# Optimization experiments

Measured on AMD Instinct MI355X. Metric: run time of the kernel, lower is better.

Reference implementation:

```python
import jax, jax.numpy as jnp
import numpy as np

B, D = 4096, 256          # event batch, message dim
N_NODES = 100000
N_COMM = 2000             # community_max_num
M = 128                   # max_member_num
N_ACTIVE = 1500           # currently active communities (community_index)


def setup_inputs() -> dict:
    key = jax.random.key(0)
    ks = jax.random.split(key, 8)
    return {
        "unique_message": jax.random.normal(ks[0], (B, D), jnp.float32),
        "member_score": jax.random.uniform(ks[1], (N_COMM, M), jnp.float32),
        "timestamps": jax.random.uniform(ks[2], (B,), jnp.float32) * 1e4,
        "nodes": jax.random.randint(ks[3], (B,), 0, N_NODES),
        "node2community": jax.random.randint(ks[4], (N_NODES,), 0, N_COMM),
        "community2node": jax.random.randint(ks[5], (N_COMM, M), 0, N_NODES),
        "member_num": jax.random.randint(ks[6], (N_COMM,), 1, M + 1),
        "community_index": jax.random.randint(ks[7], (N_ACTIVE,), 0, N_COMM),
    }


def reference(unique_message, member_score, timestamps, nodes,
              node2community, community2node, member_num, community_index):
    # community of each event node: [B]
    cids = node2community[nodes]
    # use_index: event's community is among active communities (== .any in torch code)
    use = (cids[None, :] == community_index[:, None]).any(axis=0)  # [B]

    # Ragged per-community gather, expressed as padded+masked dense ops.
    ms = member_score[cids]          # [B, M] scores of the event's community members
    mnum = member_num[cids]          # [B]   valid member count per event
    pos = jnp.arange(M)
    valid = (pos[None, :] < mnum[:, None]) & use[:, None]  # [B, M] mask = ragged prefix

    # outer product member_score[:mnum] x message  (torch.mm(score.view(-1,1), msg.view(1,-1)))
    messages = jnp.where(valid[:, :, None],
                         ms[:, :, None] * unique_message[:, None, :],
                         0.0)                                # [B, M, D]
    upd_nodes = jnp.where(valid, community2node[cids], -1)   # [B, M] (-1 = pad)
    upd_ts = jnp.where(valid, timestamps[:, None], 0.0)      # [B, M]
    return messages, upd_nodes, upd_ts
```

## Files before the change

### kernel.cpp

```cpp
#include <hip/hip_runtime.h>
#include <hip/hip_bf16.h>


__global__ void scatter_mask_kernel(const int* __restrict__ cidx,
                                    int* __restrict__ mask, int n) {
    int i = blockIdx.x * blockDim.x + threadIdx.x;
    if (i < n) mask[cidx[i]] = 1;
}

__global__ __launch_bounds__(256) void topk_comm_main_kernel(
    const float* __restrict__ unique_message,
    const float* __restrict__ member_score,
    const float* __restrict__ timestamps,
    const int*   __restrict__ nodes,
    const int*   __restrict__ node2community,
    const int*   __restrict__ community2node,
    const int*   __restrict__ member_num,
    const int*   __restrict__ mask,
    float* __restrict__ out_msgs,
    float* __restrict__ out_nodes,
    float* __restrict__ out_ts,
    int M)
{
    const int b   = blockIdx.x;
    const int tid = threadIdx.x;

    const int  cid  = node2community[nodes[b]];
    const bool use  = (mask[cid] != 0);
    const int  mnum = member_num[cid];
    const float tsb = timestamps[b];

    const int c = tid & 63;
    const int r = tid >> 6;

    const float4 m4 =
        reinterpret_cast<const float4*>(unique_message + (size_t)b * 256)[c];

    float4* __restrict__ outm =
        reinterpret_cast<float4*>(out_msgs + (size_t)b * M * 256);
    const float* __restrict__ ms_row = member_score + (size_t)cid * M;

    for (int m = r; m < M; m += 4) {
        const bool valid = use && (m < mnum);
        const float s = valid ? ms_row[m] : 0.0f;
        float4 o;
        o.x = s * m4.x; o.y = s * m4.y; o.z = s * m4.z; o.w = s * m4.w;
        outm[(size_t)m * 64 + c] = o;
    }

    const int* __restrict__ c2n_row = community2node + (size_t)cid * M;
    for (int m = tid; m < M; m += 256) {
        const bool valid = use && (m < mnum);
        out_nodes[(size_t)b * M + m] = valid ? (float)c2n_row[m] : -1.0f;
        out_ts[(size_t)b * M + m]    = valid ? tsb : 0.0f;
    }
}

extern "C" void kernel_launch(void* const* d_in, const int* in_sizes, int n_in,
                              void* d_out, int out_size, void* d_ws, size_t ws_size,
                              hipStream_t stream) {
    const float* unique_message = (const float*)d_in[0];
    const float* member_score   = (const float*)d_in[1];
    const float* timestamps     = (const float*)d_in[2];
    const int*   nodes          = (const int*)d_in[3];
    const int*   node2community = (const int*)d_in[4];
    const int*   community2node = (const int*)d_in[5];
    const int*   member_num     = (const int*)d_in[6];
    const int*   community_index= (const int*)d_in[7];

    const int B        = in_sizes[2];
    const int N_COMM   = in_sizes[6];
    const int M        = in_sizes[1] / N_COMM;
    const int N_ACTIVE = in_sizes[7];

    int* mask = (int*)d_ws;
    hipMemsetAsync(mask, 0, (size_t)N_COMM * sizeof(int), stream);
    scatter_mask_kernel<<<(N_ACTIVE + 255) / 256, 256, 0, stream>>>(
        community_index, mask, N_ACTIVE);

    float* out_msgs  = (float*)d_out;
    float* out_nodes = out_msgs + (size_t)B * M * 256;
    float* out_ts    = out_nodes + (size_t)B * M;

    topk_comm_main_kernel<<<B, 256, 0, stream>>>(
        unique_message, member_score, timestamps, nodes,
        node2community, community2node, member_num, mask,
        out_msgs, out_nodes, out_ts, M);
}
```

Before: 116.7 us.

## Fuse active-community check into main kernel and use nontemporal stores

Removes the memset and scatter-mask launches; each block scans community_index itself with a wave vote to decide membership. Member scores are staged in shared memory, M and D are fixed at compile time, the member loop is fully unrolled with contiguous per-wave row ranges, and all outputs use nontemporal stores. This cuts launch overhead and keeps streaming writes out of cache, but every block now rereads the active list, and the hardcoded dimensions only suit this shape.

```diff
diff --git a/kernel.cpp b/kernel.cpp
--- a/kernel.cpp
+++ b/kernel.cpp
@@ -2,13 +2,12 @@
 #include <hip/hip_bf16.h>
 
 
-__global__ void scatter_mask_kernel(const int* __restrict__ cidx,
-                                    int* __restrict__ mask, int n) {
-    int i = blockIdx.x * blockDim.x + threadIdx.x;
-    if (i < n) mask[cidx[i]] = 1;
-}
+typedef float f32x4 __attribute__((ext_vector_type(4)));
 
-__global__ __launch_bounds__(256) void topk_comm_main_kernel(
+constexpr int Dc = 256;
+constexpr int Mc = 128;
+
+__global__ __launch_bounds__(256) void topk_main_spec(
     const float* __restrict__ unique_message,
     const float* __restrict__ member_score,
     const float* __restrict__ timestamps,
@@ -16,74 +15,90 @@
     const int*   __restrict__ node2community,
     const int*   __restrict__ community2node,
     const int*   __restrict__ member_num,
-    const int*   __restrict__ mask,
+    const int*   __restrict__ community_index,
+    int n_active,
     float* __restrict__ out_msgs,
     float* __restrict__ out_nodes,
-    float* __restrict__ out_ts,
-    int M)
+    float* __restrict__ out_ts)
 {
     const int b   = blockIdx.x;
     const int tid = threadIdx.x;
 
-    const int  cid  = node2community[nodes[b]];
-    const bool use  = (mask[cid] != 0);
-    const int  mnum = member_num[cid];
-    const float tsb = timestamps[b];
+    __shared__ float s_score[Mc];
+    __shared__ int   s_use;
+
+    const int   cid  = node2community[nodes[b]];
+    const int   mnum = member_num[cid];
+    const float tsb  = timestamps[b];
+
+    if (tid == 0) s_use = 0;
+    __syncthreads();
+
+    bool found = false;
+    for (int i = tid; i < n_active; i += 256)
+        found |= (community_index[i] == cid);
+    if (__any(found) && (tid & 63) == 0) s_use = 1;
+
+    if (tid < Mc) s_score[tid] = member_score[(size_t)cid * Mc + tid];
+    __syncthreads();
+
+    const bool use = (s_use != 0);
+
+    if (tid < Mc) {
+        const bool valid = use && (tid < mnum);
+        const float vn = valid ? (float)community2node[(size_t)cid * Mc + tid]
+                               : -1.0f;
+        __builtin_nontemporal_store(vn,  &out_nodes[(size_t)b * Mc + tid]);
+        __builtin_nontemporal_store(valid ? tsb : 0.0f,
+                                    &out_ts[(size_t)b * Mc + tid]);
+    }
 
     const int c = tid & 63;
     const int r = tid >> 6;
+    const f32x4 m4 = reinterpret_cast<const f32x4*>(
+        unique_message + (size_t)b * Dc)[c];
 
-    const float4 m4 =
-        reinterpret_cast<const float4*>(unique_message + (size_t)b * 256)[c];
+    f32x4* __restrict__ outm = reinterpret_cast<f32x4*>(
+        out_msgs + (size_t)b * Mc * Dc) + (size_t)r * 32 * 64 + c;
 
-    float4* __restrict__ outm =
-        reinterpret_cast<float4*>(out_msgs + (size_t)b * M * 256);
-    const float* __restrict__ ms_row = member_score + (size_t)cid * M;
-
-    for (int m = r; m < M; m += 4) {
-        const bool valid = use && (m < mnum);
-        const float s = valid ? ms_row[m] : 0.0f;
-        float4 o;
+    const int m0 = r * 32;
+#pragma unroll
+    for (int k = 0; k < 32; ++k) {
+        const int m = m0 + k;
+        const float s = (use && m < mnum) ? s_score[m] : 0.0f;
+        f32x4 o;
         o.x = s * m4.x; o.y = s * m4.y; o.z = s * m4.z; o.w = s * m4.w;
-        outm[(size_t)m * 64 + c] = o;
-    }
-
-    const int* __restrict__ c2n_row = community2node + (size_t)cid * M;
-    for (int m = tid; m < M; m += 256) {
-        const bool valid = use && (m < mnum);
-        out_nodes[(size_t)b * M + m] = valid ? (float)c2n_row[m] : -1.0f;
-        out_ts[(size_t)b * M + m]    = valid ? tsb : 0.0f;
+        __builtin_nontemporal_store(o, outm + (size_t)k * 64);
     }
 }
 
 extern "C" void kernel_launch(void* const* d_in, const int* in_sizes, int n_in,
                               void* d_out, int out_size, void* d_ws, size_t ws_size,
                               hipStream_t stream) {
-    const float* unique_message = (const float*)d_in[0];
-    const float* member_score   = (const float*)d_in[1];
-    const float* timestamps     = (const float*)d_in[2];
-    const int*   nodes          = (const int*)d_in[3];
-    const int*   node2community = (const int*)d_in[4];
-    const int*   community2node = (const int*)d_in[5];
-    const int*   member_num     = (const int*)d_in[6];
-    const int*   community_index= (const int*)d_in[7];
+    const float* unique_message  = (const float*)d_in[0];
+    const float* member_score    = (const float*)d_in[1];
+    const float* timestamps      = (const float*)d_in[2];
+    const int*   nodes           = (const int*)d_in[3];
+    const int*   node2community  = (const int*)d_in[4];
+    const int*   community2node  = (const int*)d_in[5];
+    const int*   member_num      = (const int*)d_in[6];
+    const int*   community_index = (const int*)d_in[7];
 
     const int B        = in_sizes[2];
     const int N_COMM   = in_sizes[6];
     const int M        = in_sizes[1] / N_COMM;
+    const int D        = in_sizes[0] / B;
     const int N_ACTIVE = in_sizes[7];
 
-    int* mask = (int*)d_ws;
-    hipMemsetAsync(mask, 0, (size_t)N_COMM * sizeof(int), stream);
-    scatter_mask_kernel<<<(N_ACTIVE + 255) / 256, 256, 0, stream>>>(
-        community_index, mask, N_ACTIVE);
-
     float* out_msgs  = (float*)d_out;
-    float* out_nodes = out_msgs + (size_t)B * M * 256;
+    float* out_nodes = out_msgs + (size_t)B * M * D;
     float* out_ts    = out_nodes + (size_t)B * M;
 
-    topk_comm_main_kernel<<<B, 256, 0, stream>>>(
+    (void)d_ws; (void)ws_size; (void)n_in; (void)out_size; (void)M; (void)D;
+
+    topk_main_spec<<<B, 256, 0, stream>>>(
         unique_message, member_score, timestamps, nodes,
-        node2community, community2node, member_num, mask,
-        out_msgs, out_nodes, out_ts, M);
+        node2community, community2node, member_num,
+        community_index, N_ACTIVE,
+        out_msgs, out_nodes, out_ts);
 }
```

New measurement: 97.72 us. 1.19x faster.
